# Optimization experiments

Hardware: AMD Instinct MI355X
Metric: run time of the kernel (lower is better)

## Reference

```python
import jax, jax.numpy as jnp
import numpy as np

DIM = 512
HEADS = 8
DIM_HEAD = 64
INNER = HEADS * DIM_HEAD
B, N = 2, 2048
EPS = 1e-5


def setup_inputs() -> dict:
    key = jax.random.key(0)
    ks = jax.random.split(key, 7)
    x = jax.random.normal(ks[0], (B, N, DIM), dtype=jnp.float32)
    sph_dist = jax.random.uniform(ks[1], (N, N), dtype=jnp.float32)
    ln_g = jnp.ones((DIM,), jnp.float32) + 0.02 * jax.random.normal(ks[2], (DIM,))
    ln_b = 0.02 * jax.random.normal(ks[3], (DIM,))
    w_qkv = jax.random.normal(ks[4], (DIM, 3 * INNER), dtype=jnp.float32) / np.sqrt(DIM)
    w_out = jax.random.normal(ks[5], (INNER, DIM), dtype=jnp.float32) / np.sqrt(INNER)
    b_out = 0.02 * jax.random.normal(ks[6], (DIM,))
    return {"x": x, "sph_dist": sph_dist, "ln_g": ln_g, "ln_b": ln_b,
            "w_qkv": w_qkv, "w_out": w_out, "b_out": b_out}


def reference(x, sph_dist, ln_g, ln_b, w_qkv, w_out, b_out):
    scale = DIM_HEAD ** -0.5
    # LayerNorm over last dim
    mu = jnp.mean(x, axis=-1, keepdims=True)
    var = jnp.mean(jnp.square(x - mu), axis=-1, keepdims=True)
    xn = (x - mu) * jax.lax.rsqrt(var + EPS) * ln_g + ln_b
    # QKV projection -> [b, h, n, d]
    qkv = xn @ w_qkv  # [b, n, 3*inner]
    q, k, v = jnp.split(qkv, 3, axis=-1)
    split_heads = lambda t: t.reshape(B, N, HEADS, DIM_HEAD).transpose(0, 2, 1, 3)
    q, k, v = split_heads(q), split_heads(k), split_heads(v)
    dots = jnp.einsum('bhid,bhjd->bhij', q, k) * scale  # [b,h,n,n]
    dw = dots * (1.0 + sph_dist[None, None])
    # cross-head normalization: mean/std over head axis (std unbiased, ddof=1)
    m = jnp.mean(dw, axis=1, keepdims=True)
    sd = jnp.sqrt(jnp.sum(jnp.square(dw - m), axis=1, keepdims=True) / (HEADS - 1))
    dw = (dw - m) / sd
    attn = jax.nn.softmax(dw, axis=-1)
    out = jnp.einsum('bhij,bhjd->bhid', attn, v)
    out = out.transpose(0, 2, 1, 3).reshape(B, N, INNER)
    return out @ w_out + b_out
```

## Files before the change

kernel.cpp:

```cpp
#include <hip/hip_runtime.h>
#include <math.h>


typedef __attribute__((ext_vector_type(8))) short bf16x8;
typedef __attribute__((ext_vector_type(8))) unsigned short u16x8;
typedef __attribute__((ext_vector_type(4))) float f32x4;

constexpr int kDim = 512;
constexpr int kN = 2048;
constexpr float kEps = 1e-5f;
constexpr float kLog2e = 1.4426950408889634f;
constexpr float kShift2 = 2.6457513f * 1.4426950408889634f;

constexpr size_t OFF_XN   = 0;
constexpr size_t OFF_WQBT = 4u << 20;
constexpr size_t OFF_WOHIT = 6u << 20;
constexpr size_t OFF_WOLOT = (6u << 20) + (512u << 10);
constexpr size_t OFF_QHI  = 8u << 20;
constexpr size_t OFF_QLO  = 12u << 20;
constexpr size_t OFF_KHI  = 16u << 20;
constexpr size_t OFF_VTHI = 20u << 20;
constexpr size_t OFF_VNHI = 24u << 20;
constexpr size_t OFF_OP   = 28u << 20;
constexpr size_t OP_STRIDE = 2097152;
constexpr size_t OFF_AOHI = 0;
constexpr size_t OFF_AOLO = 8u << 20;

__device__ __forceinline__ unsigned short bf16_rne(float f) {
  unsigned int u = __float_as_uint(f);
  u += 0x7fffu + ((u >> 16) & 1u);
  return (unsigned short)(u >> 16);
}
__device__ __forceinline__ void bf16_split(float x, unsigned short& hi,
                                           unsigned short& lo) {
  unsigned int u = __float_as_uint(x);
  hi = (unsigned short)(u >> 16);
  float r = x - __uint_as_float(u & 0xffff0000u);
  lo = (unsigned short)(__float_as_uint(r) >> 16);
}
__device__ __forceinline__ f32x4 mfma16(bf16x8 a, bf16x8 b, f32x4 c) {
  return __builtin_amdgcn_mfma_f32_16x16x32_bf16(a, b, c, 0, 0, 0);
}

__global__ __launch_bounds__(256) void k_prep(const float* __restrict__ x,
    const float* __restrict__ g, const float* __restrict__ bta,
    const float* __restrict__ wqkv, const float* __restrict__ wout,
    unsigned short* __restrict__ xn, unsigned short* __restrict__ wqbt,
    unsigned short* __restrict__ wohit, unsigned short* __restrict__ wolot) {
  __shared__ unsigned short th[64][72];
  __shared__ unsigned short tl[64][72];
  const int bid = blockIdx.x;
  const int t = threadIdx.x;
  if (bid < 1024) {
    const int row = bid * 4 + (t >> 6);
    const int lane = t & 63;
    const float* xr = x + (size_t)row * kDim + lane * 8;
    float4 a = *(const float4*)xr;
    float4 b = *(const float4*)(xr + 4);
    float s = a.x + a.y + a.z + a.w + b.x + b.y + b.z + b.w;
    float q = a.x*a.x + a.y*a.y + a.z*a.z + a.w*a.w
            + b.x*b.x + b.y*b.y + b.z*b.z + b.w*b.w;
#pragma unroll
    for (int off = 1; off < 64; off <<= 1) {
      s += __shfl_xor(s, off);
      q += __shfl_xor(q, off);
    }
    const float m = s * (1.0f / kDim);
    const float inv = rsqrtf(q * (1.0f / kDim) - m * m + kEps);
    float4 ga = *(const float4*)(g + lane * 8);
    float4 gb = *(const float4*)(g + lane * 8 + 4);
    float4 ba = *(const float4*)(bta + lane * 8);
    float4 bb = *(const float4*)(bta + lane * 8 + 4);
    u16x8 o;
    o[0] = bf16_rne((a.x - m) * inv * ga.x + ba.x);
    o[1] = bf16_rne((a.y - m) * inv * ga.y + ba.y);
    o[2] = bf16_rne((a.z - m) * inv * ga.z + ba.z);
    o[3] = bf16_rne((a.w - m) * inv * ga.w + ba.w);
    o[4] = bf16_rne((b.x - m) * inv * gb.x + bb.x);
    o[5] = bf16_rne((b.y - m) * inv * gb.y + bb.y);
    o[6] = bf16_rne((b.z - m) * inv * gb.z + bb.z);
    o[7] = bf16_rne((b.w - m) * inv * gb.w + bb.w);
    *(u16x8*)(xn + (size_t)row * kDim + lane * 8) = o;
  } else if (bid < 1216) {
    const int tid = bid - 1024;
    const int k0 = (tid / 24) * 64;
    const int n0 = (tid % 24) * 64;
    const int r = t >> 2, c0 = (t & 3) * 16;
    const float* src = wqkv + (size_t)(k0 + r) * 1536 + n0 + c0;
#pragma unroll
    for (int qq = 0; qq < 2; ++qq) {
      float4 v0 = *(const float4*)(src + qq * 8);
      float4 v1 = *(const float4*)(src + qq * 8 + 4);
      u16x8 o;
      o[0] = bf16_rne(v0.x); o[1] = bf16_rne(v0.y);
      o[2] = bf16_rne(v0.z); o[3] = bf16_rne(v0.w);
      o[4] = bf16_rne(v1.x); o[5] = bf16_rne(v1.y);
      o[6] = bf16_rne(v1.z); o[7] = bf16_rne(v1.w);
      *(u16x8*)&th[r][c0 + qq * 8] = o;
    }
    __syncthreads();
#pragma unroll
    for (int qq = 0; qq < 2; ++qq) {
      u16x8 o;
#pragma unroll
      for (int e = 0; e < 8; ++e) o[e] = th[c0 + qq * 8 + e][r];
      *(u16x8*)(wqbt + (size_t)(n0 + r) * 512 + k0 + c0 + qq * 8) = o;
    }
  } else {
    const int tid = bid - 1216;
    const int k0 = (tid >> 3) * 64;
    const int n0 = (tid & 7) * 64;
    const int r = t >> 2, c0 = (t & 3) * 16;
    const float* src = wout + (size_t)(k0 + r) * 512 + n0 + c0;
#pragma unroll
    for (int qq = 0; qq < 2; ++qq) {
      float4 v0 = *(const float4*)(src + qq * 8);
      float4 v1 = *(const float4*)(src + qq * 8 + 4);
      float e8[8] = {v0.x, v0.y, v0.z, v0.w, v1.x, v1.y, v1.z, v1.w};
      u16x8 oh, ol;
#pragma unroll
      for (int e = 0; e < 8; ++e) {
        unsigned short h2, l2;
        bf16_split(e8[e], h2, l2);
        oh[e] = h2;
        ol[e] = l2;
      }
      *(u16x8*)&th[r][c0 + qq * 8] = oh;
      *(u16x8*)&tl[r][c0 + qq * 8] = ol;
    }
    __syncthreads();
#pragma unroll
    for (int qq = 0; qq < 2; ++qq) {
      u16x8 oh, ol;
#pragma unroll
      for (int e = 0; e < 8; ++e) {
        oh[e] = th[c0 + qq * 8 + e][r];
        ol[e] = tl[c0 + qq * 8 + e][r];
      }
      *(u16x8*)(wohit + (size_t)(n0 + r) * 512 + k0 + c0 + qq * 8) = oh;
      *(u16x8*)(wolot + (size_t)(n0 + r) * 512 + k0 + c0 + qq * 8) = ol;
    }
  }
}

__global__ __launch_bounds__(256, 3) void k_gemm_qkv(
    const unsigned short* __restrict__ xn, const unsigned short* __restrict__ wqbt,
    unsigned short* __restrict__ qhi, unsigned short* __restrict__ qlo,
    unsigned short* __restrict__ khi, unsigned short* __restrict__ vnhi) {
  __shared__ unsigned short Ah[64 * 40];
  __shared__ unsigned short Bh[128 * 40];
  const int t = threadIdx.x;
  const int wv = t >> 6;
  const int lane = t & 63;
  const int col = lane & 15, gq = lane >> 4;
  const int lg = (blockIdx.x & 7) * 96 + (blockIdx.x >> 3);
  const int n0 = (lg % 12) * 128;
  const int m0 = (lg / 12) * 64;
  const int ar = t >> 2, aq = (t & 3) * 8;
  const int bnr = t >> 1, bko = (t & 1) * 16;

  f32x4 acc[8];
#pragma unroll
  for (int bn = 0; bn < 8; ++bn) acc[bn] = (f32x4){0.f, 0.f, 0.f, 0.f};

  for (int k0 = 0; k0 < kDim; k0 += 32) {
    *(u16x8*)&Ah[ar * 40 + aq] =
        *(const u16x8*)(xn + (size_t)(m0 + ar) * kDim + k0 + aq);
    {
      const unsigned short* wr = wqbt + (size_t)(n0 + bnr) * 512 + k0 + bko;
      *(u16x8*)&Bh[bnr * 40 + bko] = *(const u16x8*)(wr);
      *(u16x8*)&Bh[bnr * 40 + bko + 8] = *(const u16x8*)(wr + 8);
    }
    __syncthreads();
    bf16x8 ahf = *(const bf16x8*)&Ah[(wv * 16 + col) * 40 + gq * 8];
#pragma unroll
    for (int bn = 0; bn < 8; ++bn) {
      bf16x8 bhf = *(const bf16x8*)&Bh[(bn * 16 + col) * 40 + gq * 8];
      acc[bn] = mfma16(ahf, bhf, acc[bn]);
    }
    __syncthreads();
  }
  const int which = n0 >> 9;
#pragma unroll
  for (int r = 0; r < 4; ++r) {
    const int m = m0 + wv * 16 + gq * 4 + r;
    const int bI = m >> 11, nn = m & 2047;
#pragma unroll
    for (int bn = 0; bn < 8; ++bn) {
      const int cc = (n0 & 511) + bn * 16 + col;
      const int hh = cc >> 6, d = cc & 63;
      const size_t base = ((size_t)(bI * 8 + hh) * kN + nn) * 64 + d;
      if (which == 0) {
        unsigned short hi2, lo2;
        bf16_split(acc[bn][r], hi2, lo2);
        qhi[base] = hi2;
        qlo[base] = lo2;
      } else {
        unsigned short* p = (which == 1) ? khi : vnhi;
        p[base] = bf16_rne(acc[bn][r]);
      }
    }
  }
}

__global__ __launch_bounds__(256) void k_vtrans(
    const unsigned short* __restrict__ vnhi, unsigned short* __restrict__ vthi) {
  __shared__ unsigned short tile[64][72];
  const int id = blockIdx.x;
  const int bh = id >> 5;
  const int nt = id & 31;
  const unsigned short* src = vnhi + ((size_t)bh * kN + nt * 64) * 64;
  unsigned short* dst = vthi + (size_t)bh * 64 * kN + nt * 64;
  const int r = threadIdx.x >> 3;
  const int c = (threadIdx.x & 7) * 8;
#pragma unroll
  for (int rr = 0; rr < 64; rr += 32) {
    u16x8 v = *(const u16x8*)(src + (size_t)(r + rr) * 64 + c);
    *(u16x8*)&tile[r + rr][c] = v;
  }
  __syncthreads();
#pragma unroll
  for (int dd = 0; dd < 64; dd += 32) {
    int d = r + dd;
    u16x8 v;
#pragma unroll
    for (int e = 0; e < 8; ++e) v[e] = tile[c + e][d];
    *(u16x8*)(dst + (size_t)d * kN + c) = v;
  }
}

__global__ __launch_bounds__(512, 2) void k_attn(
    const unsigned short* __restrict__ qhi, const unsigned short* __restrict__ qlo,
    const unsigned short* __restrict__ khi, const unsigned short* __restrict__ vthi,
    float* __restrict__ op, float* __restrict__ lsum, int jLen) {
  constexpr int SSTR = 33;
  __shared__ float Ss[2][512 * SSTR];

  const int t = threadIdx.x;
  const int h = t >> 6;
  const int lane = t & 63;
  const int col = lane & 15;
  const int g = lane >> 4;
  const int lbid = (blockIdx.x & 7) * ((int)gridDim.x >> 3) + (blockIdx.x >> 3);
  const int tileId = lbid & 63;
  const int sId = lbid >> 6;
  const int bI = tileId >> 5;
  const int i0 = (tileId & 31) << 6;
  const int jStart = sId * jLen;
  int jEnd = jStart + jLen;
  if (jEnd > kN) jEnd = kN;
  const int ntile = (jEnd - jStart) >> 5;
  const size_t bh = (size_t)bI * 8 + h;
  float* opart = op + (size_t)sId * OP_STRIDE;

  bf16x8 qhf[4][2], qlf[4][2];
#pragma unroll
  for (int rb = 0; rb < 4; ++rb) {
    const size_t qoff = (bh * kN + i0 + rb * 16 + col) * 64 + g * 8;
    qhf[rb][0] = *(const bf16x8*)(qhi + qoff);
    qhf[rb][1] = *(const bf16x8*)(qhi + qoff + 32);
    qlf[rb][0] = *(const bf16x8*)(qlo + qoff);
    qlf[rb][1] = *(const bf16x8*)(qlo + qoff + 32);
  }
  const unsigned short* kb_h = khi + (bh * kN + col) * 64 + g * 8;
  const unsigned short* vb_h = vthi + (bh * 64 + col) * kN + g * 8;

  const int iN = t >> 3;
  const int jN = (t & 7) * 4;

  f32x4 oacc[4][4];
#pragma unroll
  for (int rb = 0; rb < 4; ++rb)
#pragma unroll
    for (int nf = 0; nf < 4; ++nf) oacc[rb][nf] = (f32x4){0.f, 0.f, 0.f, 0.f};
  float lacc[8] = {0.f, 0.f, 0.f, 0.f, 0.f, 0.f, 0.f, 0.f};

  bf16x8 kh[2][2];
  auto load_k = [&](int j0) {
    const size_t ko = (size_t)j0 * 64;
#pragma unroll
    for (int jf = 0; jf < 2; ++jf)
#pragma unroll
      for (int c = 0; c < 2; ++c)
        kh[jf][c] = *(const bf16x8*)(kb_h + ko + jf * 1024 + c * 32);
  };
  auto qk_tile = [&](int buf) {
#pragma unroll
    for (int rb = 0; rb < 4; ++rb)
#pragma unroll
      for (int jf = 0; jf < 2; ++jf) {
        f32x4 a = (f32x4){0.f, 0.f, 0.f, 0.f};
        a = mfma16(qhf[rb][0], kh[jf][0], a);
        a = mfma16(qhf[rb][1], kh[jf][1], a);
        a = mfma16(qlf[rb][0], kh[jf][0], a);
        a = mfma16(qlf[rb][1], kh[jf][1], a);
#pragma unroll
        for (int r = 0; r < 4; ++r)
          Ss[buf][(h * 64 + rb * 16 + g * 4 + r) * SSTR + jf * 16 + col] = a[r];
      }
  };

  load_k(jStart);
  qk_tile(0);
  if (ntile > 1) load_k(jStart + 32);
  __syncthreads();

  for (int tt = 0; tt < ntile; ++tt) {
    const int cur = tt & 1;
    const int j0 = jStart + (tt << 5);
    if (tt + 1 < ntile) {
      qk_tile(cur ^ 1);
      if (tt + 2 < ntile) load_k(j0 + 64);
    }
    bf16x8 vhf[4];
#pragma unroll
    for (int nf = 0; nf < 4; ++nf)
      vhf[nf] = *(const bf16x8*)(vb_h + (size_t)(nf * 16) * kN + j0);
    {
      float dv[8][4];
#pragma unroll
      for (int hh = 0; hh < 8; ++hh) {
        float4 v = *(const float4*)&Ss[cur][(hh * 64 + iN) * SSTR + jN];
        dv[hh][0] = v.x; dv[hh][1] = v.y; dv[hh][2] = v.z; dv[hh][3] = v.w;
      }
#pragma unroll
      for (int jj = 0; jj < 4; ++jj) {
        float s = 0.f;
#pragma unroll
        for (int hh = 0; hh < 8; ++hh) s += dv[hh][jj];
        const float mean = s * 0.125f;
        float var = 0.f;
#pragma unroll
        for (int hh = 0; hh < 8; ++hh) {
          float d = dv[hh][jj] - mean;
          var += d * d;
        }
        const float inv2 = rsqrtf(var * (1.0f / 7.0f)) * kLog2e;
        const float base = mean * inv2 + kShift2;
#pragma unroll
        for (int hh = 0; hh < 8; ++hh)
          dv[hh][jj] = __builtin_amdgcn_exp2f(dv[hh][jj] * inv2 - base);
      }
#pragma unroll
      for (int hh = 0; hh < 8; ++hh) {
        lacc[hh] += (dv[hh][0] + dv[hh][1]) + (dv[hh][2] + dv[hh][3]);
        unsigned int p0 = (unsigned int)bf16_rne(dv[hh][0]) |
                          ((unsigned int)bf16_rne(dv[hh][1]) << 16);
        unsigned int p1 = (unsigned int)bf16_rne(dv[hh][2]) |
                          ((unsigned int)bf16_rne(dv[hh][3]) << 16);
        *(uint2*)((unsigned int*)&Ss[cur][(hh * 64 + iN) * SSTR] + (jN >> 1)) =
            make_uint2(p0, p1);
      }
    }
    __syncthreads();
    bf16x8 ph[4];
#pragma unroll
    for (int rb = 0; rb < 4; ++rb)
      ph[rb] = *(const bf16x8*)(
          (const unsigned int*)&Ss[cur][(h * 64 + rb * 16 + col) * SSTR] + g * 4);
#pragma unroll
    for (int rb = 0; rb < 4; ++rb)
#pragma unroll
      for (int nf = 0; nf < 4; ++nf)
        oacc[rb][nf] = mfma16(ph[rb], vhf[nf], oacc[rb][nf]);
    __syncthreads();
  }
#pragma unroll
  for (int off = 1; off < 8; off <<= 1)
#pragma unroll
    for (int hh = 0; hh < 8; ++hh) lacc[hh] += __shfl_xor(lacc[hh], off);
  if ((t & 7) == 0) {
#pragma unroll
    for (int hh = 0; hh < 8; ++hh)
      lsum[((size_t)sId * 16 + bI * 8 + hh) * kN + (i0 + iN)] = lacc[hh];
  }
#pragma unroll
  for (int rb = 0; rb < 4; ++rb) {
#pragma unroll
    for (int r = 0; r < 4; ++r) {
      float* dst = opart + ((size_t)bI * kN + i0 + rb * 16 + g * 4 + r) * 512 + h * 64;
#pragma unroll
      for (int nf = 0; nf < 4; ++nf)
        dst[nf * 16 + col] = oacc[rb][nf][r];
    }
  }
}

__global__ __launch_bounds__(256) void k_combine(const float* __restrict__ op,
    const float* __restrict__ lsum, int S,
    unsigned short* __restrict__ aohi, unsigned short* __restrict__ aolo) {
  const size_t e = ((size_t)blockIdx.x * 256 + threadIdx.x) * 4;
  const int row = (int)(e >> 9);
  const int col = (int)(e & 511);
  const int h = col >> 6;
  const int bI = row >> 11;
  const int n = row & 2047;
  const size_t base = (size_t)(bI * 8 + h) * kN + n;
  float L = 0.f;
  for (int s = 0; s < S; ++s) L += lsum[(size_t)s * 16 * kN + base];
  float4 acc = make_float4(0.f, 0.f, 0.f, 0.f);
  for (int s = 0; s < S; ++s) {
    float4 o4 = *(const float4*)(op + (size_t)s * OP_STRIDE + e);
    acc.x += o4.x; acc.y += o4.y; acc.z += o4.z; acc.w += o4.w;
  }
  const float inv = 1.0f / L;
  ushort4 hh, ll;
  bf16_split(acc.x * inv, hh.x, ll.x);
  bf16_split(acc.y * inv, hh.y, ll.y);
  bf16_split(acc.z * inv, hh.z, ll.z);
  bf16_split(acc.w * inv, hh.w, ll.w);
  *(ushort4*)(aohi + e) = hh;
  *(ushort4*)(aolo + e) = ll;
}

__global__ __launch_bounds__(256, 3) void k_gemm_out(
    const unsigned short* __restrict__ aohi, const unsigned short* __restrict__ aolo,
    const unsigned short* __restrict__ wohit, const unsigned short* __restrict__ wolot,
    const float* __restrict__ bias, float* __restrict__ out) {
  __shared__ unsigned short Ah[64 * 40], Al[64 * 40];
  __shared__ unsigned short Bh[128 * 40], Bl[128 * 40];
  const int t = threadIdx.x;
  const int wv = t >> 6;
  const int lane = t & 63;
  const int col = lane & 15, gq = lane >> 4;
  const int lg = (blockIdx.x & 7) * 32 + (blockIdx.x >> 3);
  const int n0 = (lg & 3) * 128;
  const int m0 = (lg >> 2) * 64;
  const int ar = t >> 2, aq = (t & 3) * 8;
  const int bnr = t >> 1, bko = (t & 1) * 16;

  f32x4 acc[8];
#pragma unroll
  for (int bn = 0; bn < 8; ++bn) acc[bn] = (f32x4){0.f, 0.f, 0.f, 0.f};

  for (int k0 = 0; k0 < 512; k0 += 32) {
    *(u16x8*)&Ah[ar * 40 + aq] =
        *(const u16x8*)(aohi + (size_t)(m0 + ar) * 512 + k0 + aq);
    *(u16x8*)&Al[ar * 40 + aq] =
        *(const u16x8*)(aolo + (size_t)(m0 + ar) * 512 + k0 + aq);
    {
      const unsigned short* wh = wohit + (size_t)(n0 + bnr) * 512 + k0 + bko;
      const unsigned short* wl = wolot + (size_t)(n0 + bnr) * 512 + k0 + bko;
      *(u16x8*)&Bh[bnr * 40 + bko] = *(const u16x8*)(wh);
      *(u16x8*)&Bh[bnr * 40 + bko + 8] = *(const u16x8*)(wh + 8);
      *(u16x8*)&Bl[bnr * 40 + bko] = *(const u16x8*)(wl);
      *(u16x8*)&Bl[bnr * 40 + bko + 8] = *(const u16x8*)(wl + 8);
    }
    __syncthreads();
    bf16x8 ahf = *(const bf16x8*)&Ah[(wv * 16 + col) * 40 + gq * 8];
    bf16x8 alf = *(const bf16x8*)&Al[(wv * 16 + col) * 40 + gq * 8];
#pragma unroll
    for (int bn = 0; bn < 8; ++bn) {
      bf16x8 bhf = *(const bf16x8*)&Bh[(bn * 16 + col) * 40 + gq * 8];
      bf16x8 blf = *(const bf16x8*)&Bl[(bn * 16 + col) * 40 + gq * 8];
      f32x4 aa = acc[bn];
      aa = mfma16(ahf, bhf, aa);
      aa = mfma16(alf, bhf, aa);
      aa = mfma16(ahf, blf, aa);
      acc[bn] = aa;
    }
    __syncthreads();
  }
  float bv[8];
#pragma unroll
  for (int bn = 0; bn < 8; ++bn) bv[bn] = bias[n0 + bn * 16 + col];
#pragma unroll
  for (int r = 0; r < 4; ++r) {
    const int m = m0 + wv * 16 + gq * 4 + r;
#pragma unroll
    for (int bn = 0; bn < 8; ++bn)
      out[(size_t)m * 512 + n0 + bn * 16 + col] = acc[bn][r] + bv[bn];
  }
}

extern "C" void kernel_launch(void* const* d_in, const int* in_sizes, int n_in,
                              void* d_out, int out_size, void* d_ws, size_t ws_size,
                              hipStream_t stream) {
  (void)in_sizes; (void)n_in; (void)out_size;
  const float* x    = (const float*)d_in[0];
  const float* g    = (const float*)d_in[2];
  const float* bta  = (const float*)d_in[3];
  const float* wqkv = (const float*)d_in[4];
  const float* wout = (const float*)d_in[5];
  const float* bout = (const float*)d_in[6];
  float* out = (float*)d_out;
  char* ws = (char*)d_ws;

  unsigned short* xn    = (unsigned short*)(ws + OFF_XN);
  unsigned short* wqbt  = (unsigned short*)(ws + OFF_WQBT);
  unsigned short* wohit = (unsigned short*)(ws + OFF_WOHIT);
  unsigned short* wolot = (unsigned short*)(ws + OFF_WOLOT);
  unsigned short* qhi   = (unsigned short*)(ws + OFF_QHI);
  unsigned short* qlo   = (unsigned short*)(ws + OFF_QLO);
  unsigned short* khi   = (unsigned short*)(ws + OFF_KHI);
  unsigned short* vthi  = (unsigned short*)(ws + OFF_VTHI);
  unsigned short* vnhi  = (unsigned short*)(ws + OFF_VNHI);
  unsigned short* aohi  = (unsigned short*)(ws + OFF_AOHI);
  unsigned short* aolo  = (unsigned short*)(ws + OFF_AOLO);
  float* op = (float*)(ws + OFF_OP);

  int S, jLen;
  if      (ws_size >= (62u << 20)) { S = 4; jLen = 512;  }
  else if (ws_size >= (53u << 20)) { S = 3; jLen = 704;  }
  else if (ws_size >= (45u << 20)) { S = 2; jLen = 1024; }
  else                             { S = 1; jLen = 2048; }
  float* lsum = (float*)(ws + OFF_OP + (size_t)S * OP_STRIDE * 4);

  k_prep<<<dim3(1280), dim3(256), 0, stream>>>(x, g, bta, wqkv, wout,
                                               xn, wqbt, wohit, wolot);
  k_gemm_qkv<<<dim3(768), dim3(256), 0, stream>>>(xn, wqbt, qhi, qlo, khi, vnhi);
  k_vtrans<<<dim3(512), dim3(256), 0, stream>>>(vnhi, vthi);
  k_attn<<<dim3(64 * S), dim3(512), 0, stream>>>(qhi, qlo, khi, vthi,
                                                 op, lsum, jLen);
  k_combine<<<dim3(2048), dim3(256), 0, stream>>>(op, lsum, S, aohi, aolo);
  k_gemm_out<<<dim3(256), dim3(256), 0, stream>>>(aohi, aolo, wohit, wolot,
                                                  bout, out);
}
```

Baseline: 124.9 us.

## Fuse V transpose into QKV GEMM epilogue and drop Q low-precision split

The V transpose now happens inside the QKV GEMM epilogue through a shared-memory tile written directly to the transposed layout, which removes the separate k_vtrans kernel launch and the intermediate V buffer. Q is stored as a single bf16 value instead of a hi/lo pair, which halves the QK^T MFMA count and the Q loads in the attention kernel. The workspace layout shrinks, so the split-count thresholds are lowered accordingly. Using bf16-only Q lowers the precision of the attention scores. The cross-head normalization may amplify this error.

Result: faster. 116.1 us (-7.1%).

```diff
diff --git a/kernel.cpp b/kernel.cpp
--- a/kernel.cpp
+++ b/kernel.cpp
@@ -12,19 +12,17 @@
 constexpr float kLog2e = 1.4426950408889634f;
 constexpr float kShift2 = 2.6457513f * 1.4426950408889634f;
 
-constexpr size_t OFF_XN   = 0;
-constexpr size_t OFF_WQBT = 4u << 20;
+constexpr size_t OFF_XN    = 0;
+constexpr size_t OFF_WQBT  = 4u << 20;
 constexpr size_t OFF_WOHIT = 6u << 20;
 constexpr size_t OFF_WOLOT = (6u << 20) + (512u << 10);
-constexpr size_t OFF_QHI  = 8u << 20;
-constexpr size_t OFF_QLO  = 12u << 20;
-constexpr size_t OFF_KHI  = 16u << 20;
-constexpr size_t OFF_VTHI = 20u << 20;
-constexpr size_t OFF_VNHI = 24u << 20;
-constexpr size_t OFF_OP   = 28u << 20;
+constexpr size_t OFF_QB    = 8u << 20;
+constexpr size_t OFF_KHI   = 12u << 20;
+constexpr size_t OFF_VTHI  = 16u << 20;
+constexpr size_t OFF_OP    = 20u << 20;
 constexpr size_t OP_STRIDE = 2097152;
-constexpr size_t OFF_AOHI = 0;
-constexpr size_t OFF_AOLO = 8u << 20;
+constexpr size_t OFF_AOHI  = 0;
+constexpr size_t OFF_AOLO  = 8u << 20;
 
 __device__ __forceinline__ unsigned short bf16_rne(float f) {
   unsigned int u = __float_as_uint(f);
@@ -145,10 +143,11 @@
 
 __global__ __launch_bounds__(256, 3) void k_gemm_qkv(
     const unsigned short* __restrict__ xn, const unsigned short* __restrict__ wqbt,
-    unsigned short* __restrict__ qhi, unsigned short* __restrict__ qlo,
-    unsigned short* __restrict__ khi, unsigned short* __restrict__ vnhi) {
+    unsigned short* __restrict__ qb, unsigned short* __restrict__ khi,
+    unsigned short* __restrict__ vthi) {
   __shared__ unsigned short Ah[64 * 40];
   __shared__ unsigned short Bh[128 * 40];
+  __shared__ unsigned short Vt[128 * 72];
   const int t = threadIdx.x;
   const int wv = t >> 6;
   const int lane = t & 63;
@@ -181,57 +180,40 @@
     __syncthreads();
   }
   const int which = n0 >> 9;
-#pragma unroll
-  for (int r = 0; r < 4; ++r) {
-    const int m = m0 + wv * 16 + gq * 4 + r;
-    const int bI = m >> 11, nn = m & 2047;
-#pragma unroll
-    for (int bn = 0; bn < 8; ++bn) {
-      const int cc = (n0 & 511) + bn * 16 + col;
-      const int hh = cc >> 6, d = cc & 63;
-      const size_t base = ((size_t)(bI * 8 + hh) * kN + nn) * 64 + d;
-      if (which == 0) {
-        unsigned short hi2, lo2;
-        bf16_split(acc[bn][r], hi2, lo2);
-        qhi[base] = hi2;
-        qlo[base] = lo2;
-      } else {
-        unsigned short* p = (which == 1) ? khi : vnhi;
-        p[base] = bf16_rne(acc[bn][r]);
-      }
-    }
-  }
-}
-
-__global__ __launch_bounds__(256) void k_vtrans(
-    const unsigned short* __restrict__ vnhi, unsigned short* __restrict__ vthi) {
-  __shared__ unsigned short tile[64][72];
-  const int id = blockIdx.x;
-  const int bh = id >> 5;
-  const int nt = id & 31;
-  const unsigned short* src = vnhi + ((size_t)bh * kN + nt * 64) * 64;
-  unsigned short* dst = vthi + (size_t)bh * 64 * kN + nt * 64;
-  const int r = threadIdx.x >> 3;
-  const int c = (threadIdx.x & 7) * 8;
-#pragma unroll
-  for (int rr = 0; rr < 64; rr += 32) {
-    u16x8 v = *(const u16x8*)(src + (size_t)(r + rr) * 64 + c);
-    *(u16x8*)&tile[r + rr][c] = v;
-  }
-  __syncthreads();
-#pragma unroll
-  for (int dd = 0; dd < 64; dd += 32) {
-    int d = r + dd;
-    u16x8 v;
-#pragma unroll
-    for (int e = 0; e < 8; ++e) v[e] = tile[c + e][d];
-    *(u16x8*)(dst + (size_t)d * kN + c) = v;
+  if (which < 2) {
+    unsigned short* p = (which == 0) ? qb : khi;
+#pragma unroll
+    for (int r = 0; r < 4; ++r) {
+      const int m = m0 + wv * 16 + gq * 4 + r;
+      const int bI = m >> 11, nn = m & 2047;
+#pragma unroll
+      for (int bn = 0; bn < 8; ++bn) {
+        const int cc = (n0 & 511) + bn * 16 + col;
+        const int hh = cc >> 6, d = cc & 63;
+        p[((size_t)(bI * 8 + hh) * kN + nn) * 64 + d] = bf16_rne(acc[bn][r]);
+      }
+    }
+  } else {
+#pragma unroll
+    for (int bn = 0; bn < 8; ++bn)
+#pragma unroll
+      for (int r = 0; r < 4; ++r)
+        Vt[(bn * 16 + col) * 72 + wv * 16 + gq * 4 + r] = bf16_rne(acc[bn][r]);
+    __syncthreads();
+    const int cl = t >> 1, mo = (t & 1) * 32;
+    const int cc = (n0 & 511) + cl;
+    const int hh = cc >> 6, d = cc & 63;
+    const int bI = m0 >> 11, ntok = (m0 & 2047) + mo;
+    unsigned short* dst = vthi + ((size_t)(bI * 8 + hh) * 64 + d) * kN + ntok;
+#pragma unroll
+    for (int e = 0; e < 4; ++e)
+      *(u16x8*)(dst + e * 8) = *(const u16x8*)&Vt[cl * 72 + mo + e * 8];
   }
 }
 
 __global__ __launch_bounds__(512, 2) void k_attn(
-    const unsigned short* __restrict__ qhi, const unsigned short* __restrict__ qlo,
-    const unsigned short* __restrict__ khi, const unsigned short* __restrict__ vthi,
+    const unsigned short* __restrict__ qb, const unsigned short* __restrict__ khi,
+    const unsigned short* __restrict__ vthi,
     float* __restrict__ op, float* __restrict__ lsum, int jLen) {
   constexpr int SSTR = 33;
   __shared__ float Ss[2][512 * SSTR];
@@ -253,14 +235,12 @@
   const size_t bh = (size_t)bI * 8 + h;
   float* opart = op + (size_t)sId * OP_STRIDE;
 
-  bf16x8 qhf[4][2], qlf[4][2];
+  bf16x8 qhf[4][2];
 #pragma unroll
   for (int rb = 0; rb < 4; ++rb) {
     const size_t qoff = (bh * kN + i0 + rb * 16 + col) * 64 + g * 8;
-    qhf[rb][0] = *(const bf16x8*)(qhi + qoff);
-    qhf[rb][1] = *(const bf16x8*)(qhi + qoff + 32);
-    qlf[rb][0] = *(const bf16x8*)(qlo + qoff);
-    qlf[rb][1] = *(const bf16x8*)(qlo + qoff + 32);
+    qhf[rb][0] = *(const bf16x8*)(qb + qoff);
+    qhf[rb][1] = *(const bf16x8*)(qb + qoff + 32);
   }
   const unsigned short* kb_h = khi + (bh * kN + col) * 64 + g * 8;
   const unsigned short* vb_h = vthi + (bh * 64 + col) * kN + g * 8;
@@ -292,8 +272,6 @@
         f32x4 a = (f32x4){0.f, 0.f, 0.f, 0.f};
         a = mfma16(qhf[rb][0], kh[jf][0], a);
         a = mfma16(qhf[rb][1], kh[jf][1], a);
-        a = mfma16(qlf[rb][0], kh[jf][0], a);
-        a = mfma16(qlf[rb][1], kh[jf][1], a);
 #pragma unroll
         for (int r = 0; r < 4; ++r)
           Ss[buf][(h * 64 + rb * 16 + g * 4 + r) * SSTR + jf * 16 + col] = a[r];
@@ -490,28 +468,24 @@
   unsigned short* wqbt  = (unsigned short*)(ws + OFF_WQBT);
   unsigned short* wohit = (unsigned short*)(ws + OFF_WOHIT);
   unsigned short* wolot = (unsigned short*)(ws + OFF_WOLOT);
-  unsigned short* qhi   = (unsigned short*)(ws + OFF_QHI);
-  unsigned short* qlo   = (unsigned short*)(ws + OFF_QLO);
+  unsigned short* qb    = (unsigned short*)(ws + OFF_QB);
   unsigned short* khi   = (unsigned short*)(ws + OFF_KHI);
   unsigned short* vthi  = (unsigned short*)(ws + OFF_VTHI);
-  unsigned short* vnhi  = (unsigned short*)(ws + OFF_VNHI);
   unsigned short* aohi  = (unsigned short*)(ws + OFF_AOHI);
   unsigned short* aolo  = (unsigned short*)(ws + OFF_AOLO);
   float* op = (float*)(ws + OFF_OP);
 
   int S, jLen;
-  if      (ws_size >= (62u << 20)) { S = 4; jLen = 512;  }
-  else if (ws_size >= (53u << 20)) { S = 3; jLen = 704;  }
-  else if (ws_size >= (45u << 20)) { S = 2; jLen = 1024; }
+  if      (ws_size >= (54u << 20)) { S = 4; jLen = 512;  }
+  else if (ws_size >= (46u << 20)) { S = 3; jLen = 704;  }
+  else if (ws_size >= (37u << 20)) { S = 2; jLen = 1024; }
   else                             { S = 1; jLen = 2048; }
   float* lsum = (float*)(ws + OFF_OP + (size_t)S * OP_STRIDE * 4);
 
   k_prep<<<dim3(1280), dim3(256), 0, stream>>>(x, g, bta, wqkv, wout,
                                                xn, wqbt, wohit, wolot);
-  k_gemm_qkv<<<dim3(768), dim3(256), 0, stream>>>(xn, wqbt, qhi, qlo, khi, vnhi);
-  k_vtrans<<<dim3(512), dim3(256), 0, stream>>>(vnhi, vthi);
-  k_attn<<<dim3(64 * S), dim3(512), 0, stream>>>(qhi, qlo, khi, vthi,
-                                                 op, lsum, jLen);
+  k_gemm_qkv<<<dim3(768), dim3(256), 0, stream>>>(xn, wqbt, qb, khi, vthi);
+  k_attn<<<dim3(64 * S), dim3(512), 0, stream>>>(qb, khi, vthi, op, lsum, jLen);
   k_combine<<<dim3(2048), dim3(256), 0, stream>>>(op, lsum, S, aohi, aolo);
   k_gemm_out<<<dim3(256), dim3(256), 0, stream>>>(aohi, aolo, wohit, wolot,
                                                   bout, out);
```
